# Kernel tuning notes

Measured on AMD Instinct MI355X. Metric: run time of the kernel, lower is better.

The kernel has to match this reference:

```python
import jax, jax.numpy as jnp
import numpy as np

B, Lc, Le, H, V = 128, 512, 512, 512, 128
PAD_IDX = 0  # ignore_index for cross entropy


def _lstm_cell(x, h, c, Wih, Whh, bih, bhh):
    # PyTorch gate order: i, f, g, o
    gates = x @ Wih.T + h @ Whh.T + bih + bhh
    i, f, g, o = jnp.split(gates, 4, axis=-1)
    c_new = jax.nn.sigmoid(f) * c + jax.nn.sigmoid(i) * jnp.tanh(g)
    h_new = jax.nn.sigmoid(o) * jnp.tanh(c_new)
    return h_new, c_new


def setup_inputs() -> dict:
    key = jax.random.key(0)
    ks = jax.random.split(key, 16)
    s = 0.05  # weight init scale
    inp = {
        "C": jax.random.normal(ks[0], (B, Lc, V), jnp.float32),
        "C_pad": jax.random.randint(ks[1], (B, Lc), 0, 2, jnp.int32).at[:, 0].set(0),
        "E": jax.random.randint(ks[2], (B, Le), 0, V, jnp.int32),
        "E_emb": jax.random.normal(ks[3], (B, Le, V), jnp.float32),
        # encoder LSTM (input V -> hidden H)
        "enc_Wih": s * jax.random.normal(ks[4], (4 * H, V), jnp.float32),
        "enc_Whh": s * jax.random.normal(ks[5], (4 * H, H), jnp.float32),
        "enc_bih": jnp.zeros((4 * H,), jnp.float32),
        "enc_bhh": jnp.zeros((4 * H,), jnp.float32),
        # decoder LSTMCell (input V+H -> hidden H); input is concat([E_emb_t, V_prev])
        "dec_Wih": s * jax.random.normal(ks[6], (4 * H, V + H), jnp.float32),
        "dec_Whh": s * jax.random.normal(ks[7], (4 * H, H), jnp.float32),
        "dec_bih": jnp.zeros((4 * H,), jnp.float32),
        "dec_bhh": jnp.zeros((4 * H,), jnp.float32),
        # attention_proj: Linear(H, H, bias=False)
        "att_W": s * jax.random.normal(ks[8], (H, H), jnp.float32),
        # output_proj: Linear(2H, H)
        "out_W": s * jax.random.normal(ks[9], (H, 2 * H), jnp.float32),
        "out_b": jnp.zeros((H,), jnp.float32),
        # vocab_proj: Linear(H, V)
        "voc_W": s * jax.random.normal(ks[10], (V, H), jnp.float32),
        "voc_b": jnp.zeros((V,), jnp.float32),
    }
    return inp


def reference(C, C_pad, E, E_emb, enc_Wih, enc_Whh, enc_bih, enc_bhh,
              dec_Wih, dec_Whh, dec_bih, dec_bhh, att_W, out_W, out_b,
              voc_W, voc_b):
    Bv = C.shape[0]
    Hh = enc_Whh.shape[1]

    # ---- encoder LSTM over compressed input ----
    def enc_step(carry, x_t):
        h, c = carry
        h, c = _lstm_cell(x_t, h, c, enc_Wih, enc_Whh, enc_bih, enc_bhh)
        return (h, c), h

    h0 = jnp.zeros((Bv, Hh), C.dtype)
    (hT, cT), enc_hs = jax.lax.scan(enc_step, (h0, h0), jnp.swapaxes(C, 0, 1))
    enc_hs = jnp.swapaxes(enc_hs, 0, 1)  # (B, Lc, H)
    pad = C_pad.astype(bool)              # (B, Lc)

    # ---- decoder loop (training mode, teacher forcing) ----
    def dec_step(carry, e_t):
        h, c, Vprev = carry
        x = jnp.concatenate([e_t, Vprev], axis=1)  # (B, V+H)
        h, c = _lstm_cell(x, h, c, dec_Wih, dec_Whh, dec_bih, dec_bhh)
        q = h @ att_W.T                                    # (B, H)
        scores = jnp.einsum('blh,bh->bl', enc_hs, q)       # (B, Lc)
        scores = jnp.where(pad, -jnp.inf, scores)
        d = jax.nn.softmax(scores, axis=1)
        attn = jnp.einsum('bl,blh->bh', d, enc_hs)         # (B, H)
        U = jnp.concatenate([h, attn], axis=1)             # (B, 2H)
        Vnew = U @ out_W.T + out_b                         # (B, H)
        # dropout treated as identity (eval-mode determinism)
        logits = jnp.tanh(Vnew) @ voc_W.T + voc_b          # (B, V)
        return (h, c, Vnew), logits

    Vinit = jnp.zeros((Bv, Hh), C.dtype)
    _, logits = jax.lax.scan(dec_step, (hT, cT, Vinit),
                             jnp.swapaxes(E_emb[:, :-1], 0, 1))
    logits = jnp.swapaxes(logits, 0, 1)  # (B, Le-1, V)

    # ---- cross entropy with ignore_index=PAD_IDX ----
    targets = E[:, 1:].astype(jnp.int32)
    logp = jax.nn.log_softmax(logits, axis=-1)
    nll = -jnp.take_along_axis(logp, targets[..., None], axis=-1)[..., 0]
    mask = (targets != PAD_IDX).astype(nll.dtype)
    loss = jnp.sum(nll * mask) / jnp.maximum(jnp.sum(mask), 1.0)
    return loss
```

## Files before the change

### kernel.cpp

```cpp
#include <hip/hip_runtime.h>
#include <hip/hip_bf16.h>


#define NWG 256
#define NT  256

typedef unsigned short u16;
typedef unsigned int   u32;
typedef unsigned long long u64;
typedef __attribute__((ext_vector_type(4))) float f4;
typedef __attribute__((ext_vector_type(8))) short s8;

constexpr int Bv=128, Lc=512, Le=512, Hd=512, Vc=128;
constexpr int KE=640, KD=1152;
constexpr int CAP = 144;
constexpr int SPN = 24;

constexpr size_t O_WENC = 8192;
constexpr size_t O_WDEC = O_WENC + (size_t)2048*KE*2;
constexpr size_t O_WDF  = O_WDEC + (size_t)2048*KD*2;
constexpr size_t O_ATWT = O_WDF  + (size_t)2048*KD*2;
constexpr size_t O_OUTW = O_ATWT + (size_t)512*512*2;
constexpr size_t O_VOCW = O_OUTW + (size_t)512*1024*2;
constexpr size_t O_BE   = O_VOCW + (size_t)128*512*2;
constexpr size_t O_BD   = O_BE + 8192;
constexpr size_t O_BDF  = O_BD + 8192;
constexpr size_t O_H    = O_BDF + 8192;
constexpr size_t O_TNH  = O_H + (size_t)2*128*512*2;
constexpr size_t O_PFX  = O_TNH + (size_t)2*128*512*2;
constexpr size_t O_CNT  = O_PFX + (size_t)128*512*4;
constexpr size_t O_PMS  = O_CNT + 512;
constexpr size_t O_PACC = O_PMS + 2048;
constexpr size_t O_REC  = O_PACC + (size_t)256*512*2;
constexpr size_t O_LOSS = O_REC + (size_t)2*128*2*4*4;
constexpr size_t O_ENC  = O_LOSS + 256;
constexpr size_t O_PSP  = O_ENC + (size_t)128*512*512*2;
constexpr size_t O_CST  = O_PSP + (size_t)256*SPN*512*2;

constexpr int SC       = CAP*1024;
constexpr int SM_BYTES = SC + 16384;

struct P {
  const float *C; const int *Cpad; const int *E; const float *Eemb;
  const float *eWih,*eWhh,*ebih,*ebhh;
  const float *dWih,*dWhh,*dbih,*dbhh;
  const float *attW,*outW,*outb,*vocW,*vocb;
  char* ws; float* out;
};

__device__ inline u16 f2bf(float x){
  u32 u = __float_as_uint(x);
  return (u16)((u + 0x7fffu + ((u>>16)&1u)) >> 16);
}
__device__ inline float bf2f(u16 b){ return __uint_as_float(((u32)b)<<16); }
__device__ inline float sigm(float x){ return 1.f/(1.f+expf(-x)); }
__device__ inline f4 MM(s8 a, s8 b, f4 c){
  return __builtin_amdgcn_mfma_f32_16x16x32_bf16(a, b, c, 0, 0, 0);
}
__device__ inline u64 ld64a(const void* p){
  return __hip_atomic_load((const u64*)p, __ATOMIC_RELAXED, __HIP_MEMORY_SCOPE_AGENT);
}
__device__ inline u32 ld32u(const void* p){
  return __hip_atomic_load((const u32*)p, __ATOMIC_RELAXED, __HIP_MEMORY_SCOPE_AGENT);
}
__device__ inline void st64a(void* p, u64 v){
  __hip_atomic_store((u64*)p, v, __ATOMIC_RELAXED, __HIP_MEMORY_SCOPE_AGENT);
}
__device__ inline void st32a(void* p, u32 v){
  __hip_atomic_store((u32*)p, v, __ATOMIC_RELAXED, __HIP_MEMORY_SCOPE_AGENT);
}
__device__ inline s8 ld16a(const void* p){
  union { u64 q[2]; s8 v; } u;
  u.q[0] = ld64a(p); u.q[1] = ld64a((const char*)p + 8);
  return u.v;
}
__device__ inline s8 cvt8(const float* p){
  f4 u = *(const f4*)p, v = *(const f4*)(p+4);
  s8 r;
  r[0]=(short)f2bf(u[0]); r[1]=(short)f2bf(u[1]); r[2]=(short)f2bf(u[2]); r[3]=(short)f2bf(u[3]);
  r[4]=(short)f2bf(v[0]); r[5]=(short)f2bf(v[1]); r[6]=(short)f2bf(v[2]); r[7]=(short)f2bf(v[3]);
  return r;
}
__device__ inline float wredmax(float v){
  #pragma unroll
  for (int m=32;m;m>>=1) v = fmaxf(v, __shfl_xor(v,m,64));
  return v;
}
__device__ inline float wredsum(float v){
  #pragma unroll
  for (int m=32;m;m>>=1) v += __shfl_xor(v,m,64);
  return v;
}

extern "C" __global__ void __launch_bounds__(NT,1) k_enc(P p)
{
  extern __shared__ char sm[];
  const int wg = blockIdx.x, tid = threadIdx.x;
  const int gt = wg*NT + tid;
  const int rg = wg >> 5, cg = wg & 31;

  char* ws = p.ws;
  u32*  slotA = (u32*)ws;
  u32*  slotR = (u32*)(ws + 1024 + rg*128);
  u16*  wenc = (u16*)(ws + O_WENC);
  u16*  wdec = (u16*)(ws + O_WDEC);
  u16*  wdf  = (u16*)(ws + O_WDF);
  u16*  atwt = (u16*)(ws + O_ATWT);
  u16*  outw = (u16*)(ws + O_OUTW);
  u16*  vocw = (u16*)(ws + O_VOCW);
  float* be  = (float*)(ws + O_BE);
  float* bd  = (float*)(ws + O_BD);
  float* bdf = (float*)(ws + O_BDF);
  u16*  hbf  = (u16*)(ws + O_H);
  u32*  pfx  = (u32*)(ws + O_PFX);
  u32*  cntp = (u32*)(ws + O_CNT);
  float* losp= (float*)(ws + O_LOSS);
  u16*  encc = (u16*)(ws + O_ENC);
  float* cstg= (float*)(ws + O_CST);

  u32 genA = 0, genG = 0;
  auto GBall = [&](){
    genA++;
    __syncthreads();
// ... 98 lines not shown
    int* padl = (int*)(sm + SC);
    for (int i = tid; i < 512; i += NT) padl[i] = p.Cpad[wg*512 + i];
    __syncthreads();
    if (tid == 0){
      u32 run = 0;
      for (int tt = 0; tt < 512; tt++){ pfx[wg*512+tt] = run; if (padl[tt] == 0) run++; }
      cntp[wg] = run;
    }
    __syncthreads();
  }
  GBall();

  const int l  = tid & 63, wv = tid >> 6;
  const int n2 = wv >> 1, k2 = wv & 1;
  const int kl = (l>>4) << 3;
  const int ar = rg*16 + (l&15);
  float cst = 0.f;

  const int gR0 = (n2*2+0)*512 + cg*16 + (l&15);
  const int gR1 = (n2*2+1)*512 + cg*16 + (l&15);

  for (int t = 0; t < Lc; t++){
    const u16* hold = hbf + (t&1)*Bv*Hd;
    u16* hnew       = hbf + ((t+1)&1)*Bv*Hd;
    s8 a[10];
    if (k2 == 0){
      #pragma unroll
      for (int ks = 4; ks < 10; ks++)
        a[ks] = ld16a(hold + (size_t)ar*Hd + (ks*32 + kl - 128));
      #pragma unroll
      for (int ks = 0; ks < 4; ks++)
        a[ks] = cvt8(p.C + ((size_t)ar*Lc + t)*Vc + ks*32 + kl);
    } else {
      #pragma unroll
      for (int ks = 0; ks < 10; ks++)
        a[ks] = ld16a(hold + (size_t)ar*Hd + (192 + ks*32 + kl));
    }
    f4 acc0 = {0,0,0,0}, acc1 = {0,0,0,0};
    #pragma unroll
    for (int ks = 0; ks < 10; ks++){
      int k = k2*320 + ks*32 + kl;
      acc0 = MM(a[ks], *(const s8*)(wenc + (size_t)gR0*KE + k), acc0);
      acc1 = MM(a[ks], *(const s8*)(wenc + (size_t)gR1*KE + k), acc1);
    }
    float* exch = (float*)(sm + SC);
    #pragma unroll
    for (int r = 0; r < 4; r++){
      int row = ((l>>4)<<2) + r;
      exch[((k2*4 + n2*2+0)*16 + row)*16 + (l&15)] = acc0[r];
      exch[((k2*4 + n2*2+1)*16 + row)*16 + (l&15)] = acc1[r];
    }
    __syncthreads();
    {
      int row = tid >> 4, u = tid & 15;
      int gb = cg*16 + u;
      float gi = exch[((0)*16+row)*16+u] + exch[((4)*16+row)*16+u] + be[0*512+gb];
      float gf = exch[((1)*16+row)*16+u] + exch[((5)*16+row)*16+u] + be[1*512+gb];
      float gg = exch[((2)*16+row)*16+u] + exch[((6)*16+row)*16+u] + be[2*512+gb];
      float go = exch[((3)*16+row)*16+u] + exch[((7)*16+row)*16+u] + be[3*512+gb];
      float fi = sigm(gi), ff = sigm(gf), fg = tanhf(gg), fo = sigm(go);
      cst = ff*cst + fi*fg;
      float hn = fo * tanhf(cst);
      int b = rg*16 + row;
      u32 hb = f2bf(hn);
      u32 nb = __shfl_xor((int)hb, 1, 64);
      if ((tid & 1) == 0){
        u32 pk = hb | (nb << 16);
        st32a(hnew + (size_t)b*Hd + gb, pk);
        if (p.Cpad[b*Lc + t] == 0){
          u32 pos = pfx[b*Lc + t];
          st32a(encc + ((size_t)b*Lc + pos)*Hd + gb, pk);
        }
      }
    }
    RGB();
  }

  {
    int row = tid >> 4, u = tid & 15;
    cstg[(size_t)(rg*16+row)*Hd + cg*16 + u] = cst;
  }
}

extern "C" __global__ void __launch_bounds__(NT,1) k_dec(P p)
{
  extern __shared__ char sm[];
  const int wg = blockIdx.x, tid = threadIdx.x;
  const int rg = wg >> 5, cg = wg & 31;

  char* ws = p.ws;
  u32*  slotA = (u32*)(ws + 2048);
  u32*  slotR = (u32*)(ws + 4096 + rg*128);
  u16*  wdec = (u16*)(ws + O_WDEC);
  u16*  wdf  = (u16*)(ws + O_WDF);
  u16*  atwt = (u16*)(ws + O_ATWT);
  u16*  outw = (u16*)(ws + O_OUTW);
  u16*  vocw = (u16*)(ws + O_VOCW);
  float* bd  = (float*)(ws + O_BD);
  float* bdf = (float*)(ws + O_BDF);
  u16*  hbf  = (u16*)(ws + O_H);
  u16*  tnhb = (u16*)(ws + O_TNH);
  u32*  cntp = (u32*)(ws + O_CNT);
  u64*  pms  = (u64*)(ws + O_PMS);
  u16*  pacc16 = (u16*)(ws + O_PACC);
  float* rec = (float*)(ws + O_REC);
  float* losp= (float*)(ws + O_LOSS);
  u16*  encc = (u16*)(ws + O_ENC);
  u16*  spl  = (u16*)(ws + O_PSP) + (size_t)wg*SPN*Hd;
  float* cstg= (float*)(ws + O_CST);

  u32 genA = 0, genG = 0;
  auto GBall = [&](){
    genA++;
    __syncthreads();
    if (tid == 0){
      __builtin_amdgcn_fence(__ATOMIC_RELEASE, "agent");
      st32a(slotA + wg, genA);
    }
    if (tid < 64){
      bool done = false;
      while (!done){
        u32 v0 = ld32u(slotA + tid);
        u32 v1 = ld32u(slotA + 64 + tid);
        u32 v2 = ld32u(slotA + 128 + tid);
        u32 v3 = ld32u(slotA + 192 + tid);
        done = __all((v0>=genA)&&(v1>=genA)&&(v2>=genA)&&(v3>=genA));
        if (!done) __builtin_amdgcn_s_sleep(4);
      }
      __builtin_amdgcn_fence(__ATOMIC_ACQUIRE, "agent");
    }
    __syncthreads();
  };
  auto RGB = [&](){
    genG++;
    __syncthreads();
    if (tid == 0) st32a(slotR + cg, genG);
    if (tid < 64){
      bool done = false;
      while (!done){
        u32 v = ld32u(slotR + (tid & 31));
        done = __all(v >= genG);
        if (!done) __builtin_amdgcn_s_sleep(2);
      }
      __builtin_amdgcn_fence(__ATOMIC_ACQUIRE, "workgroup");
    }
    __syncthreads();
  };

  const int l  = tid & 63, wv = tid >> 6;
  const int n2 = wv >> 1, k2 = wv & 1;
  const int kl = (l>>4) << 3;
  const int ar = rg*16 + (l&15);
  float accN = 0.f, accC = 0.f;

  float cst;
  {
    int row = tid >> 4, u = tid & 15;
    cst = cstg[(size_t)(rg*16+row)*Hd + cg*16 + u];
  }

  const int rowA = rg*16 + (cg >> 1), halfA = cg & 1;
  const int cnA = (int)cntp[rowA], c2A = cnA >> 1;
  const int loA = halfA ? c2A : 0;
  const int mynA = (halfA ? cnA : c2A) - loA;
  const int ncapA = mynA < CAP ? mynA : CAP;
  const int limA  = mynA < CAP+SPN ? mynA : CAP+SPN;
  u16* eP = (u16*)sm;

  auto CEREC = [&](int tl){
    u32* th16 = (u32*)(sm + SC + 11776);
    float* lgp = (float*)(sm + SC + 12800);
    float* lgh = (float*)(sm + SC + 13824);
    const u16* tb = tnhb + (size_t)(tl&1)*Bv*Hd + (size_t)rowA*Hd;
    th16[tid] = ld32u(tb + 2*tid);
    __syncthreads();
    {
      int v = tid & 63, ksl = tid >> 6;
      int gv = halfA*64 + v;
      const u16* wp = vocw + (size_t)gv*Hd + ksl*128;
      const u16* hp = (const u16*)th16 + ksl*128;
      float acc = 0.f;
      #pragma unroll 4
      for (int j = 0; j < 16; j++){
        s8 wv8 = *(const s8*)(wp + j*8);
        #pragma unroll
        for (int q = 0; q < 8; q++) acc += bf2f((u16)wv8[q]) * bf2f(hp[j*8+q]);
      }
      lgp[ksl*64 + v] = acc;
    }
    __syncthreads();
    if (tid < 64){
      int gv = halfA*64 + tid;
      float lv = lgp[tid] + lgp[64+tid] + lgp[128+tid] + lgp[192+tid] + p.vocb[gv];
      lgh[tid] = lv;
      float m = wredmax(lv);
      float s = wredsum(expf(lv - m));
      if (tid == 0){
        int tgt = p.E[rowA*Le + tl + 1];
        float tlg = (tgt >= halfA*64 && tgt < halfA*64+64) ? lgh[tgt - halfA*64] : 0.f;
        float* rp = rec + ((size_t)(tl&1)*256 + rowA*2 + halfA)*4;
        union { u64 q; float f[2]; } pk; pk.f[0]=m; pk.f[1]=s;
        st64a(rp, pk.q);
        st32a(rp+2, __float_as_uint(tlg));
      }
    }
    __syncthreads();
  };
  auto COMB = [&](int tl){
    int tgt = p.E[rowA*Le + tl + 1];
    if (tgt != 0){
      const float* rp = rec + ((size_t)(tl&1)*256 + rowA*2)*4;
      union { u64 q; float f[2]; } a, b;
      a.q = ld64a(rp); b.q = ld64a(rp+4);
      float tA = __uint_as_float(ld32u(rp+2)), tB = __uint_as_float(ld32u(rp+6));
      float M = fmaxf(a.f[0], b.f[0]);
      float S = a.f[1]*expf(a.f[0]-M) + b.f[1]*expf(b.f[0]-M);
      accN += logf(S) + M - (tA + tB);
      accC += 1.f;
    }
  };

  const int gR0 = (n2*2+0)*512 + cg*16 + (l&15);
  const int gR1 = (n2*2+1)*512 + cg*16 + (l&15);

  {
    const u16* erow = encc + ((size_t)rowA*Lc + loA)*Hd;
    for (int it = 0; it*16 < limA; it++){
      s8 afr[16];
      const u16* ap = erow + (size_t)(it*16 + (l&15))*Hd;
      #pragma unroll
      for (int ks = 0; ks < 16; ks++) afr[ks] = *(const s8*)(ap + ks*32 + kl);
      for (int ot = 0; ot < 8; ot++){
        int kout0 = wv*128 + ot*16;
        f4 acc = {0,0,0,0};
        #pragma unroll
        for (int ks = 0; ks < 16; ks++)
          acc = MM(afr[ks], *(const s8*)(atwt + (size_t)(kout0 + (l&15))*Hd + ks*32 + kl), acc);
        #pragma unroll
        for (int r = 0; r < 4; r++){
          int prow = it*16 + ((l>>4)<<2) + r;
          int pcol = kout0 + (l&15);
          if (prow < limA){
            u16 pv = f2bf(acc[r]);
            if (prow < CAP) eP[(size_t)prow*Hd + pcol] = pv;
            else            spl[(size_t)(prow-CAP)*Hd + pcol] = pv;
          }
        }
      }
    }
    __syncthreads();
  }

  float* exch = (float*)(sm + SC);
  float* vex  = (float*)(sm + SC + 8192);
  float* sc2  = (float*)(sm + SC + 12288);
  s8 aH[14];

  for (int t = 0; t < Le-1; t++){
    const u16* hold = hbf + (t&1)*Bv*Hd;
    u16* hnew       = hbf + ((t+1)&1)*Bv*Hd;

    if (t == 0){
      s8 a[10];
      #pragma unroll
      for (int ks = 0; ks < 10; ks++){
        int ke = (k2==0) ? ((ks<4) ? ks*32+kl : 640 + (ks-4)*32 + kl)
                         : (832 + ks*32 + kl);
        if (ke < 128) a[ks] = cvt8(p.Eemb + ((size_t)ar*Le + 0)*Vc + ke);
        else          a[ks] = ld16a(hold + (size_t)ar*Hd + (ke-640));
      }
      f4 acc0 = {0,0,0,0}, acc1 = {0,0,0,0};
      #pragma unroll
      for (int ks = 0; ks < 10; ks++){
        int ke = (k2==0) ? ((ks<4) ? ks*32+kl : 640 + (ks-4)*32 + kl)
                         : (832 + ks*32 + kl);
        acc0 = MM(a[ks], *(const s8*)(wdec + (size_t)gR0*KD + ke), acc0);
        acc1 = MM(a[ks], *(const s8*)(wdec + (size_t)gR1*KD + ke), acc1);
      }
      #pragma unroll
      for (int r = 0; r < 4; r++){
        int row = ((l>>4)<<2) + r;
        exch[((k2*4 + n2*2+0)*16 + row)*16 + (l&15)] = acc0[r];
        exch[((k2*4 + n2*2+1)*16 + row)*16 + (l&15)] = acc1[r];
      }
      __syncthreads();
      {
        int row = tid >> 4, u = tid & 15;
        int gb = cg*16 + u;
        float gi = exch[((0)*16+row)*16+u] + exch[((4)*16+row)*16+u] + bd[0*512+gb];
        float gf = exch[((1)*16+row)*16+u] + exch[((5)*16+row)*16+u] + bd[1*512+gb];
        float gg = exch[((2)*16+row)*16+u] + exch[((6)*16+row)*16+u] + bd[2*512+gb];
        float go = exch[((3)*16+row)*16+u] + exch[((7)*16+row)*16+u] + bd[3*512+gb];
        float fi = sigm(gi), ff = sigm(gf), fg = tanhf(gg), fo = sigm(go);
        cst = ff*cst + fi*fg;
        float hn = fo * tanhf(cst);
        u32 hb = f2bf(hn);
        u32 nb = __shfl_xor((int)hb, 1, 64);
        if ((tid & 1) == 0)
          st32a(hnew + (size_t)(rg*16+row)*Hd + gb, hb | (nb << 16));
      }
    } else {
      if (tid < 16){
        union { u64 q; float f[2]; } uA, uB;
        uA.q = ld64a(pms + (rg*16+tid)*2 + 0);
        uB.q = ld64a(pms + (rg*16+tid)*2 + 1);
        float M = fmaxf(uA.f[0], uB.f[0]);
        float eA = (uA.f[0] > -1e29f) ? expf(uA.f[0]-M) : 0.f;
        float eB = (uB.f[0] > -1e29f) ? expf(uB.f[0]-M) : 0.f;
        float den = uA.f[1]*eA + uB.f[1]*eB;
        sc2[tid*2]   = eA/den;
        sc2[tid*2+1] = eB/den;
      }
      __syncthreads();
      const int colc = cg*16 + (l&15);
      if (k2 == 0){
        s8 a[18];
        #pragma unroll
        for (int ks = 4; ks < 18; ks++) a[ks] = aH[ks-4];
        #pragma unroll
        for (int ks = 0; ks < 4; ks++)
          a[ks] = cvt8(p.Eemb + ((size_t)ar*Le + t)*Vc + ks*32 + kl);
        f4 acc0 = {0,0,0,0}, acc1 = {0,0,0,0}, vac = {0,0,0,0};
        #pragma unroll
        for (int ks = 0; ks < 18; ks++){
          int k = ks*32 + kl;
          acc0 = MM(a[ks], *(const s8*)(wdf + (size_t)gR0*KD + k), acc0);
          acc1 = MM(a[ks], *(const s8*)(wdf + (size_t)gR1*KD + k), acc1);
          int ck = ks - 4;
          if (ck >= 0 && ((ck & 1) == n2))
            vac = MM(a[ks], *(const s8*)(outw + (size_t)colc*1024 + ck*32 + kl), vac);
        }
        #pragma unroll
        for (int r = 0; r < 4; r++){
          int row = ((l>>4)<<2) + r;
          exch[((n2*2+0)*16 + row)*16 + (l&15)] = acc0[r];
          exch[((n2*2+1)*16 + row)*16 + (l&15)] = acc1[r];
          vex[wv*256 + row*16 + (l&15)] = vac[r];
        }
      } else {
        const u16* pA = pacc16 + (size_t)(ar*2+0)*Hd;
        const u16* pB = pacc16 + (size_t)(ar*2+1)*Hd;
        s8 h0f = aH[0], h1f = aH[1];
        f4 acc0 = {0,0,0,0}, acc1 = {0,0,0,0};
        f4 aA0 = {0,0,0,0}, aA1 = {0,0,0,0}, aB0 = {0,0,0,0}, aB1 = {0,0,0,0};
        f4 vH = {0,0,0,0}, vA = {0,0,0,0}, vB = {0,0,0,0};
        acc0 = MM(h0f, *(const s8*)(wdf + (size_t)gR0*KD + 576 + kl), acc0);
        acc1 = MM(h0f, *(const s8*)(wdf + (size_t)gR1*KD + 576 + kl), acc1);
        acc0 = MM(h1f, *(const s8*)(wdf + (size_t)gR0*KD + 608 + kl), acc0);
        acc1 = MM(h1f, *(const s8*)(wdf + (size_t)gR1*KD + 608 + kl), acc1);
        {
          s8 hf = (n2 == 0) ? h0f : h1f;
          vH = MM(hf, *(const s8*)(outw + (size_t)colc*1024 + (14+n2)*32 + kl), vH);
        }
        #pragma unroll
        for (int hb = 0; hb < 2; hb++){
          s8 pf[8];
          #pragma unroll
          for (int j = 0; j < 8; j++)
            pf[j] = ld16a(pA + (hb*8+j)*32 + kl);
          #pragma unroll
          for (int j = 0; j < 8; j++){
            int c = hb*8 + j;
            int k = 640 + c*32 + kl;
            aA0 = MM(pf[j], *(const s8*)(wdf + (size_t)gR0*KD + k), aA0);
            aA1 = MM(pf[j], *(const s8*)(wdf + (size_t)gR1*KD + k), aA1);
            if (((16 + c) & 1) == n2)
              vA = MM(pf[j], *(const s8*)(outw + (size_t)colc*1024 + (16+c)*32 + kl), vA);
          }
        }
        #pragma unroll
        for (int hb = 0; hb < 2; hb++){
          s8 pf[8];
          #pragma unroll
          for (int j = 0; j < 8; j++)
            pf[j] = ld16a(pB + (hb*8+j)*32 + kl);
          #pragma unroll
          for (int j = 0; j < 8; j++){
            int c = hb*8 + j;
            int k = 640 + c*32 + kl;
            aB0 = MM(pf[j], *(const s8*)(wdf + (size_t)gR0*KD + k), aB0);
            aB1 = MM(pf[j], *(const s8*)(wdf + (size_t)gR1*KD + k), aB1);
            if (((16 + c) & 1) == n2)
              vB = MM(pf[j], *(const s8*)(outw + (size_t)colc*1024 + (16+c)*32 + kl), vB);
          }
        }
        #pragma unroll
        for (int r = 0; r < 4; r++){
          int row = ((l>>4)<<2) + r;
          float sAr = sc2[row*2], sBr = sc2[row*2+1];
          exch[((4 + n2*2+0)*16 + row)*16 + (l&15)] = acc0[r] + sAr*aA0[r] + sBr*aB0[r];
          exch[((4 + n2*2+1)*16 + row)*16 + (l&15)] = acc1[r] + sAr*aA1[r] + sBr*aB1[r];
          vex[wv*256 + row*16 + (l&15)] = vH[r] + sAr*vA[r] + sBr*vB[r];
        }
      }
      __syncthreads();
      {
        int row = tid >> 4, u = tid & 15;
        int gb = cg*16 + u;
        float gi = exch[((0)*16+row)*16+u] + exch[((4)*16+row)*16+u] + bdf[0*512+gb];
        float gf = exch[((1)*16+row)*16+u] + exch[((5)*16+row)*16+u] + bdf[1*512+gb];
        float gg = exch[((2)*16+row)*16+u] + exch[((6)*16+row)*16+u] + bdf[2*512+gb];
        float go = exch[((3)*16+row)*16+u] + exch[((7)*16+row)*16+u] + bdf[3*512+gb];
        float fi = sigm(gi), ff = sigm(gf), fg = tanhf(gg), fo = sigm(go);
        cst = ff*cst + fi*fg;
        float hn = fo * tanhf(cst);
        u32 hb = f2bf(hn);
        u32 nb = __shfl_xor((int)hb, 1, 64);
        if ((tid & 1) == 0)
          st32a(hnew + (size_t)(rg*16+row)*Hd + gb, hb | (nb << 16));
        float v = vex[row*16+u] + vex[256+row*16+u] + vex[512+row*16+u]
                + vex[768+row*16+u] + p.outb[gb];
        u32 tb2 = f2bf(tanhf(v));
        u32 tn2 = __shfl_xor((int)tb2, 1, 64);
        if ((tid & 1) == 0){
          u16* tnw = tnhb + (size_t)((t-1)&1)*Bv*Hd;
          st32a(tnw + (size_t)(rg*16+row)*Hd + gb, tb2 | (tn2 << 16));
        }
      }
    }
    RGB();

    {
      const int ne = limA, ncap = ncapA;
      float* hld = (float*)(sm + SC);
      float* scl = (float*)(sm + SC + 2048);
      float* red = (float*)(sm + SC + 2816);
      float* part= (float*)(sm + SC + 3584);
      {
        u32 hw = ld32u(hnew + (size_t)rowA*Hd + 2*tid);
        int c0 = 2*tid, c1 = c0+1;
        hld[(c0&15)*32 + (c0>>4)] = bf2f((u16)(hw & 0xffffu));
        hld[(c1&15)*32 + (c1>>4)] = bf2f((u16)(hw >> 16));
      }
      __syncthreads();
      const int pg8 = tid >> 5, ln = tid & 31;
      int i = pg8;
      for (; i < ncap; i += 8){
        const u16* e = eP + (size_t)i*Hd + ln*16;
        s8 ev0 = *(const s8*)(e);
        s8 ev1 = *(const s8*)(e+8);
        float s = 0.f;
        #pragma unroll
        for (int j=0;j<8;j++) s += bf2f((u16)ev0[j]) * hld[j*32+ln];
        #pragma unroll
        for (int j=0;j<8;j++) s += bf2f((u16)ev1[j]) * hld[(j+8)*32+ln];
        #pragma unroll
        for (int m=1;m<32;m<<=1) s += __shfl_xor(s, m, 64);
        if (ln == 0) scl[i] = s;
      }
      for (; i < ne; i += 8){
        const u16* e = spl + (size_t)(i-CAP)*Hd + ln*16;
        s8 ev0 = *(const s8*)(e);
        s8 ev1 = *(const s8*)(e+8);
        float s = 0.f;
        #pragma unroll
        for (int j=0;j<8;j++) s += bf2f((u16)ev0[j]) * hld[j*32+ln];
        #pragma unroll
        for (int j=0;j<8;j++) s += bf2f((u16)ev1[j]) * hld[(j+8)*32+ln];
        #pragma unroll
        for (int m=1;m<32;m<<=1) s += __shfl_xor(s, m, 64);
        if (ln == 0) scl[i] = s;
      }
      __syncthreads();
      float mloc = -1e30f;
      for (int i2 = tid; i2 < ne; i2 += NT) mloc = fmaxf(mloc, scl[i2]);
      mloc = wredmax(mloc);
      if ((tid&63)==0) red[tid>>6] = mloc;
      __syncthreads();
      float M = fmaxf(fmaxf(red[0],red[1]), fmaxf(red[2],red[3]));
      __syncthreads();
      float sloc = 0.f;
      for (int i2 = tid; i2 < ne; i2 += NT){ float w = expf(scl[i2]-M); scl[i2]=w; sloc += w; }
      sloc = wredsum(sloc);
      if ((tid&63)==0) red[tid>>6] = sloc;
      __syncthreads();
      float S = red[0]+red[1]+red[2]+red[3];
      float a8[8] = {0,0,0,0,0,0,0,0};
      const u16* eb2 = encc + ((size_t)rowA*Lc + loA)*Hd + l*8;
      int ii = wv;
      for (; ii + 28 < ne; ii += 32){
        s8 e0 = *(const s8*)(eb2 + (size_t)(ii    )*Hd);
        s8 e1 = *(const s8*)(eb2 + (size_t)(ii+ 4)*Hd);
        s8 e2 = *(const s8*)(eb2 + (size_t)(ii+ 8)*Hd);
        s8 e3 = *(const s8*)(eb2 + (size_t)(ii+12)*Hd);
        s8 e4 = *(const s8*)(eb2 + (size_t)(ii+16)*Hd);
        s8 e5 = *(const s8*)(eb2 + (size_t)(ii+20)*Hd);
        s8 e6 = *(const s8*)(eb2 + (size_t)(ii+24)*Hd);
        s8 e7 = *(const s8*)(eb2 + (size_t)(ii+28)*Hd);
        float w0=scl[ii], w1=scl[ii+4], w2=scl[ii+8], w3=scl[ii+12];
        float w4=scl[ii+16], w5=scl[ii+20], w6=scl[ii+24], w7=scl[ii+28];
        #pragma unroll
        for (int j=0;j<8;j++) a8[j] += w0*bf2f((u16)e0[j]) + w1*bf2f((u16)e1[j])
                                    + w2*bf2f((u16)e2[j]) + w3*bf2f((u16)e3[j])
                                    + w4*bf2f((u16)e4[j]) + w5*bf2f((u16)e5[j])
                                    + w6*bf2f((u16)e6[j]) + w7*bf2f((u16)e7[j]);
      }
      for (; ii < ne; ii += 4){
        s8 e0 = *(const s8*)(eb2 + (size_t)ii*Hd);
        float w0 = scl[ii];
        #pragma unroll
        for (int j=0;j<8;j++) a8[j] += w0*bf2f((u16)e0[j]);
      }
      { f4 v0 = {a8[0],a8[1],a8[2],a8[3]}, v1 = {a8[4],a8[5],a8[6],a8[7]};
        *(f4*)(part + wv*512 + l*8)     = v0;
        *(f4*)(part + wv*512 + l*8 + 4) = v1; }
      __syncthreads();
      {
        int h0 = 2*tid;
        float a0 = part[h0] + part[512+h0] + part[1024+h0] + part[1536+h0];
        float a1 = part[h0+1] + part[512+h0+1] + part[1024+h0+1] + part[1536+h0+1];
        st32a(pacc16 + (size_t)(rowA*2+halfA)*Hd + h0, (u32)f2bf(a0) | ((u32)f2bf(a1) << 16));
        if (tid == 0){
          union { u64 q; float f[2]; } pk; pk.f[0]=M; pk.f[1]=S;
          st64a(pms + rowA*2 + halfA, pk.q);
        }
      }
      __syncthreads();
      if (t >= 1) CEREC(t-1);
      if (t >= 2 && halfA == 0 && tid == 0) COMB(t-2);
      if (t < Le-2){
        if (k2 == 0){
          #pragma unroll
          for (int ks = 4; ks < 18; ks++)
            aH[ks-4] = ld16a(hnew + (size_t)ar*Hd + (ks*32 + kl - 128));
        } else {
          aH[0] = ld16a(hnew + (size_t)ar*Hd + (448 + kl));
          aH[1] = ld16a(hnew + (size_t)ar*Hd + (480 + kl));
        }
      }
    }
    RGB();
  }

  const int TL = Le-2;
  {
    if (tid < 16){
      union { u64 q; float f[2]; } uA, uB;
      uA.q = ld64a(pms + (rg*16+tid)*2 + 0);
      uB.q = ld64a(pms + (rg*16+tid)*2 + 1);
      float M = fmaxf(uA.f[0], uB.f[0]);
      float eA = (uA.f[0] > -1e29f) ? expf(uA.f[0]-M) : 0.f;
      float eB = (uB.f[0] > -1e29f) ? expf(uB.f[0]-M) : 0.f;
      float den = uA.f[1]*eA + uB.f[1]*eB;
      sc2[tid*2]   = eA/den;
      sc2[tid*2+1] = eB/den;
    }
    __syncthreads();
    const float scA = sc2[(l&15)*2], scB = sc2[(l&15)*2+1];
    const u16* h5 = hbf + (size_t)((TL+1)&1)*Bv*Hd;
    const u16* pA = pacc16 + (size_t)(ar*2+0)*Hd;
    const u16* pB = pacc16 + (size_t)(ar*2+1)*Hd;
    const int colc = cg*16 + (l&15);
    f4 vac = {0,0,0,0};
    #pragma unroll
    for (int j = 0; j < 8; j++){
      int kv = k2*16 + j*2 + n2;
      s8 af;
      if (kv < 16) af = ld16a(h5 + (size_t)ar*Hd + kv*32 + kl);
      else {
        s8 va = ld16a(pA + (kv-16)*32 + kl);
        s8 vb = ld16a(pB + (kv-16)*32 + kl);
        #pragma unroll
        for (int q = 0; q < 8; q++)
          af[q] = (short)f2bf(scA*bf2f((u16)va[q]) + scB*bf2f((u16)vb[q]));
      }
      vac = MM(af, *(const s8*)(outw + (size_t)colc*1024 + kv*32 + kl), vac);
    }
    #pragma unroll
    for (int r = 0; r < 4; r++)
      vex[wv*256 + (((l>>4)<<2)+r)*16 + (l&15)] = vac[r];
    __syncthreads();
    {
      int row = tid >> 4, u = tid & 15;
      int gb = cg*16 + u;
      float v = vex[row*16+u] + vex[256+row*16+u] + vex[512+row*16+u]
              + vex[768+row*16+u] + p.outb[gb];
      u32 tb2 = f2bf(tanhf(v));
      u32 tn2 = __shfl_xor((int)tb2, 1, 64);
      if ((tid & 1) == 0){
        u16* tnw = tnhb + (size_t)(TL&1)*Bv*Hd;
        st32a(tnw + (size_t)(rg*16+row)*Hd + gb, tb2 | (tn2 << 16));
      }
    }
  }
  RGB();
  {
    CEREC(TL);
    if (halfA == 0 && tid == 0) COMB(TL-1);
  }
  RGB();
  {
    if (halfA == 0 && tid == 0){
      COMB(TL);
      atomicAdd(losp + 0, accN);
      atomicAdd(losp + 1, accC);
    }
  }
  GBall();
  if (wg == 0 && tid == 0) p.out[0] = losp[0] / fmaxf(losp[1], 1.f);
}

extern "C" void kernel_launch(void* const* d_in, const int* in_sizes, int n_in,
                              void* d_out, int out_size, void* d_ws, size_t ws_size,
                              hipStream_t stream)
{
  hipFuncSetAttribute(reinterpret_cast<const void*>(k_enc),
                      hipFuncAttributeMaxDynamicSharedMemorySize, SM_BYTES);
  hipFuncSetAttribute(reinterpret_cast<const void*>(k_dec),
                      hipFuncAttributeMaxDynamicSharedMemorySize, SM_BYTES);
  hipMemsetAsync(d_ws, 0, 8192, stream);

  P prm;
  prm.C    = (const float*)d_in[0];
  prm.Cpad = (const int*)  d_in[1];
  prm.E    = (const int*)  d_in[2];
  prm.Eemb = (const float*)d_in[3];
  prm.eWih = (const float*)d_in[4];
  prm.eWhh = (const float*)d_in[5];
  prm.ebih = (const float*)d_in[6];
  prm.ebhh = (const float*)d_in[7];
  prm.dWih = (const float*)d_in[8];
  prm.dWhh = (const float*)d_in[9];
  prm.dbih = (const float*)d_in[10];
  prm.dbhh = (const float*)d_in[11];
  prm.attW = (const float*)d_in[12];
  prm.outW = (const float*)d_in[13];
  prm.outb = (const float*)d_in[14];
  prm.vocW = (const float*)d_in[15];
  prm.vocb = (const float*)d_in[16];
  prm.ws   = (char*)d_ws;
  prm.out  = (float*)d_out;

  k_enc<<<dim3(NWG), dim3(NT), SM_BYTES, stream>>>(prm);
  k_dec<<<dim3(NWG), dim3(NT), SM_BYTES, stream>>>(prm);
}
```

Baseline: 21.57 ms.

## Split decoder across 512 workgroups with 4-way attention partitioning per row

The decoder kernel now launches 512 persistent workgroups (two per CU via launch_bounds) instead of 256. Each row-group covers 8 batch rows instead of 16, and the attention over encoder states for each row is split four ways instead of two. The per-workgroup LDS cache of encoder projections shrinks to fit two blocks per CU. The partial softmax, attention and cross-entropy combines are widened to merge four partials. This spreads the attention and vocab work over more CUs, at the cost of a grid barrier that polls 512 slots, redundant MFMA tiles where only 8 of 16 rows are valid, and more spill to global memory.

```diff
diff --git a/kernel.cpp b/kernel.cpp
--- a/kernel.cpp
+++ b/kernel.cpp
@@ -4,6 +4,7 @@
 
 #define NWG 256
 #define NT  256
+#define NWG2 512
 
 typedef unsigned short u16;
 typedef unsigned int   u32;
@@ -13,8 +14,8 @@
 
 constexpr int Bv=128, Lc=512, Le=512, Hd=512, Vc=128;
 constexpr int KE=640, KD=1152;
-constexpr int CAP = 144;
-constexpr int SPN = 24;
+constexpr int CAP2 = 60;
+constexpr int SPN2 = 24;
 
 constexpr size_t O_WENC = 8192;
 constexpr size_t O_WDEC = O_WENC + (size_t)2048*KE*2;
@@ -30,15 +31,17 @@
 constexpr size_t O_PFX  = O_TNH + (size_t)2*128*512*2;
 constexpr size_t O_CNT  = O_PFX + (size_t)128*512*4;
 constexpr size_t O_PMS  = O_CNT + 512;
-constexpr size_t O_PACC = O_PMS + 2048;
-constexpr size_t O_REC  = O_PACC + (size_t)256*512*2;
-constexpr size_t O_LOSS = O_REC + (size_t)2*128*2*4*4;
+constexpr size_t O_PACC = O_PMS + 4096;
+constexpr size_t O_REC  = O_PACC + (size_t)128*4*512*2;
+constexpr size_t O_LOSS = O_REC + 16384;
 constexpr size_t O_ENC  = O_LOSS + 256;
 constexpr size_t O_PSP  = O_ENC + (size_t)128*512*512*2;
-constexpr size_t O_CST  = O_PSP + (size_t)256*SPN*512*2;
-
-constexpr int SC       = CAP*1024;
+constexpr size_t O_CST  = O_PSP + (size_t)NWG2*SPN2*512*2;
+
+constexpr int SC       = 144*1024;
 constexpr int SM_BYTES = SC + 16384;
+constexpr int SC2       = CAP2*1024;
+constexpr int SM2_BYTES = SC2 + 16384;
 
 struct P {
   const float *C; const int *Cpad; const int *E; const float *Eemb;
@@ -303,15 +306,15 @@
   }
 }
 
-extern "C" __global__ void __launch_bounds__(NT,1) k_dec(P p)
+extern "C" __global__ void __launch_bounds__(NT,2) k_dec(P p)
 {
   extern __shared__ char sm[];
   const int wg = blockIdx.x, tid = threadIdx.x;
-  const int rg = wg >> 5, cg = wg & 31;
+  const int rgx = wg >> 5, cg = wg & 31;
 
   char* ws = p.ws;
   u32*  slotA = (u32*)(ws + 2048);
-  u32*  slotR = (u32*)(ws + 4096 + rg*128);
+  u32*  slotR = (u32*)(ws + 4096 + rgx*128);
   u16*  wdec = (u16*)(ws + O_WDEC);
   u16*  wdf  = (u16*)(ws + O_WDF);
   u16*  atwt = (u16*)(ws + O_ATWT);
@@ -327,7 +330,7 @@
   float* rec = (float*)(ws + O_REC);
   float* losp= (float*)(ws + O_LOSS);
   u16*  encc = (u16*)(ws + O_ENC);
-  u16*  spl  = (u16*)(ws + O_PSP) + (size_t)wg*SPN*Hd;
+  u16*  spl  = (u16*)(ws + O_PSP) + (size_t)wg*SPN2*Hd;
   float* cstg= (float*)(ws + O_CST);
 
   u32 genA = 0, genG = 0;
@@ -341,11 +344,11 @@
     if (tid < 64){
       bool done = false;
       while (!done){
-        u32 v0 = ld32u(slotA + tid);
-        u32 v1 = ld32u(slotA + 64 + tid);
-        u32 v2 = ld32u(slotA + 128 + tid);
-        u32 v3 = ld32u(slotA + 192 + tid);
-        done = __all((v0>=genA)&&(v1>=genA)&&(v2>=genA)&&(v3>=genA));
+        bool ok = true;
+        #pragma unroll
+        for (int i = 0; i < 8; i++)
+          ok = ok && (ld32u(slotA + tid + 64*i) >= genA);
+        done = __all(ok);
         if (!done) __builtin_amdgcn_s_sleep(4);
       }
       __builtin_amdgcn_fence(__ATOMIC_ACQUIRE, "agent");
@@ -371,55 +374,62 @@
   const int l  = tid & 63, wv = tid >> 6;
   const int n2 = wv >> 1, k2 = wv & 1;
   const int kl = (l>>4) << 3;
-  const int ar = rg*16 + (l&15);
+  const int ar = rgx*8 + (l&7);
   float accN = 0.f, accC = 0.f;
 
-  float cst;
-  {
+  float cst = 0.f;
+  if (tid < 128){
     int row = tid >> 4, u = tid & 15;
-    cst = cstg[(size_t)(rg*16+row)*Hd + cg*16 + u];
-  }
-
-  const int rowA = rg*16 + (cg >> 1), halfA = cg & 1;
-  const int cnA = (int)cntp[rowA], c2A = cnA >> 1;
-  const int loA = halfA ? c2A : 0;
-  const int mynA = (halfA ? cnA : c2A) - loA;
-  const int ncapA = mynA < CAP ? mynA : CAP;
-  const int limA  = mynA < CAP+SPN ? mynA : CAP+SPN;
+    cst = cstg[(size_t)(rgx*8+row)*Hd + cg*16 + u];
+  }
+
+  const int rowA = rgx*8 + (cg >> 2), q4 = cg & 3;
+  const int cnA = (int)cntp[rowA];
+  const int loA = (cnA * q4) >> 2;
+  const int hiA = (cnA * (q4+1)) >> 2;
+  const int mynA = hiA - loA;
+  const int ncapA = mynA < CAP2 ? mynA : CAP2;
+  const int limA  = mynA < CAP2+SPN2 ? mynA : CAP2+SPN2;
   u16* eP = (u16*)sm;
 
   auto CEREC = [&](int tl){
-    u32* th16 = (u32*)(sm + SC + 11776);
-    float* lgp = (float*)(sm + SC + 12800);
-    float* lgh = (float*)(sm + SC + 13824);
+    u32* th16 = (u32*)(sm + SC2 + 11776);
+    float* lgp = (float*)(sm + SC2 + 12800);
+    float* lgh = (float*)(sm + SC2 + 13824);
     const u16* tb = tnhb + (size_t)(tl&1)*Bv*Hd + (size_t)rowA*Hd;
     th16[tid] = ld32u(tb + 2*tid);
     __syncthreads();
     {
-      int v = tid & 63, ksl = tid >> 6;
-      int gv = halfA*64 + v;
-      const u16* wp = vocw + (size_t)gv*Hd + ksl*128;
-      const u16* hp = (const u16*)th16 + ksl*128;
+      int v = tid & 31, ksl = tid >> 5;
+      int gv = q4*32 + v;
+      const u16* wp = vocw + (size_t)gv*Hd + ksl*64;
+      const u16* hp = (const u16*)th16 + ksl*64;
       float acc = 0.f;
-      #pragma unroll 4
-      for (int j = 0; j < 16; j++){
+      #pragma unroll
+      for (int j = 0; j < 8; j++){
         s8 wv8 = *(const s8*)(wp + j*8);
         #pragma unroll
         for (int q = 0; q < 8; q++) acc += bf2f((u16)wv8[q]) * bf2f(hp[j*8+q]);
       }
-      lgp[ksl*64 + v] = acc;
-    }
-    __syncthreads();
-    if (tid < 64){
-      int gv = halfA*64 + tid;
-      float lv = lgp[tid] + lgp[64+tid] + lgp[128+tid] + lgp[192+tid] + p.vocb[gv];
+      lgp[ksl*32 + v] = acc;
+    }
+    __syncthreads();
+    if (tid < 32){
+      int gv = q4*32 + tid;
+      float lv = p.vocb[gv];
+      #pragma unroll
+      for (int s2 = 0; s2 < 8; s2++) lv += lgp[s2*32 + tid];
       lgh[tid] = lv;
-      float m = wredmax(lv);
-      float s = wredsum(expf(lv - m));
+      float m = lv, s;
+      #pragma unroll
+      for (int mk=16;mk;mk>>=1) m = fmaxf(m, __shfl_xor(m, mk, 64));
+      s = expf(lv - m);
+      #pragma unroll
+      for (int mk=16;mk;mk>>=1) s += __shfl_xor(s, mk, 64);
       if (tid == 0){
         int tgt = p.E[rowA*Le + tl + 1];
-        float tlg = (tgt >= halfA*64 && tgt < halfA*64+64) ? lgh[tgt - halfA*64] : 0.f;
-        float* rp = rec + ((size_t)(tl&1)*256 + rowA*2 + halfA)*4;
+        float tlg = (tgt >= q4*32 && tgt < q4*32+32) ? lgh[tgt - q4*32] : 0.f;
+        float* rp = rec + ((size_t)(tl&1)*2048 + rowA*16 + q4*4);
         union { u64 q; float f[2]; } pk; pk.f[0]=m; pk.f[1]=s;
         st64a(rp, pk.q);
         st32a(rp+2, __float_as_uint(tlg));
@@ -430,13 +440,21 @@
   auto COMB = [&](int tl){
     int tgt = p.E[rowA*Le + tl + 1];
     if (tgt != 0){
-      const float* rp = rec + ((size_t)(tl&1)*256 + rowA*2)*4;
-      union { u64 q; float f[2]; } a, b;
-      a.q = ld64a(rp); b.q = ld64a(rp+4);
-      float tA = __uint_as_float(ld32u(rp+2)), tB = __uint_as_float(ld32u(rp+6));
-      float M = fmaxf(a.f[0], b.f[0]);
-      float S = a.f[1]*expf(a.f[0]-M) + b.f[1]*expf(b.f[0]-M);
-      accN += logf(S) + M - (tA + tB);
+      const float* rp = rec + ((size_t)(tl&1)*2048 + rowA*16);
+      float m[4], s[4], tsum = 0.f;
+      #pragma unroll
+      for (int q = 0; q < 4; q++){
+        union { u64 u; float f[2]; } a;
+        a.u = ld64a(rp + q*4);
+        m[q] = a.f[0]; s[q] = a.f[1];
+        tsum += __uint_as_float(ld32u(rp + q*4 + 2));
+      }
+      float M = fmaxf(fmaxf(m[0],m[1]), fmaxf(m[2],m[3]));
+      float S = 0.f;
+      #pragma unroll
+      for (int q = 0; q < 4; q++)
+        S += (m[q] > -1e29f) ? s[q]*expf(m[q]-M) : 0.f;
+      accN += logf(S) + M - tsum;
       accC += 1.f;
     }
   };
@@ -463,8 +481,8 @@
           int pcol = kout0 + (l&15);
           if (prow < limA){
             u16 pv = f2bf(acc[r]);
-            if (prow < CAP) eP[(size_t)prow*Hd + pcol] = pv;
-            else            spl[(size_t)(prow-CAP)*Hd + pcol] = pv;
+            if (prow < CAP2) eP[(size_t)prow*Hd + pcol] = pv;
+            else             spl[(size_t)(prow-CAP2)*Hd + pcol] = pv;
           }
         }
       }
@@ -472,9 +490,9 @@
     __syncthreads();
   }
 
-  float* exch = (float*)(sm + SC);
-  float* vex  = (float*)(sm + SC + 8192);
-  float* sc2  = (float*)(sm + SC + 12288);
+  float* exch = (float*)(sm + SC2);
+  float* vex  = (float*)(sm + SC2 + 8192);
+  float* sc4  = (float*)(sm + SC2 + 12288);
   s8 aH[14];
 
   for (int t = 0; t < Le-1; t++){
@@ -505,7 +523,7 @@
         exch[((k2*4 + n2*2+1)*16 + row)*16 + (l&15)] = acc1[r];
       }
       __syncthreads();
-      {
+      if (tid < 128){
         int row = tid >> 4, u = tid & 15;
         int gb = cg*16 + u;
         float gi = exch[((0)*16+row)*16+u] + exch[((4)*16+row)*16+u] + bd[0*512+gb];
@@ -518,19 +536,26 @@
         u32 hb = f2bf(hn);
         u32 nb = __shfl_xor((int)hb, 1, 64);
         if ((tid & 1) == 0)
-          st32a(hnew + (size_t)(rg*16+row)*Hd + gb, hb | (nb << 16));
+          st32a(hnew + (size_t)(rgx*8+row)*Hd + gb, hb | (nb << 16));
       }
     } else {
-      if (tid < 16){
-        union { u64 q; float f[2]; } uA, uB;
-        uA.q = ld64a(pms + (rg*16+tid)*2 + 0);
-        uB.q = ld64a(pms + (rg*16+tid)*2 + 1);
-        float M = fmaxf(uA.f[0], uB.f[0]);
-        float eA = (uA.f[0] > -1e29f) ? expf(uA.f[0]-M) : 0.f;
-        float eB = (uB.f[0] > -1e29f) ? expf(uB.f[0]-M) : 0.f;
-        float den = uA.f[1]*eA + uB.f[1]*eB;
-        sc2[tid*2]   = eA/den;
-        sc2[tid*2+1] = eB/den;
+      if (tid < 8){
+        float m[4], s[4];
+        #pragma unroll
+        for (int q = 0; q < 4; q++){
+          union { u64 u; float f[2]; } a;
+          a.u = ld64a(pms + (rgx*8+tid)*4 + q);
+          m[q] = a.f[0]; s[q] = a.f[1];
+        }
+        float M = fmaxf(fmaxf(m[0],m[1]), fmaxf(m[2],m[3]));
+        float e[4]; float den = 0.f;
+        #pragma unroll
+        for (int q = 0; q < 4; q++){
+          e[q] = (m[q] > -1e29f) ? expf(m[q]-M) : 0.f;
+          den += s[q]*e[q];
+        }
+        #pragma unroll
+        for (int q = 0; q < 4; q++) sc4[tid*4+q] = e[q]/den;
       }
       __syncthreads();
       const int colc = cg*16 + (l&15);
@@ -559,12 +584,15 @@
           vex[wv*256 + row*16 + (l&15)] = vac[r];
         }
       } else {
-        const u16* pA = pacc16 + (size_t)(ar*2+0)*Hd;
-        const u16* pB = pacc16 + (size_t)(ar*2+1)*Hd;
+        const u16* pQ0 = pacc16 + (size_t)(ar*4+0)*Hd;
+        const u16* pQ1 = pacc16 + (size_t)(ar*4+1)*Hd;
+        const u16* pQ2 = pacc16 + (size_t)(ar*4+2)*Hd;
+        const u16* pQ3 = pacc16 + (size_t)(ar*4+3)*Hd;
         s8 h0f = aH[0], h1f = aH[1];
         f4 acc0 = {0,0,0,0}, acc1 = {0,0,0,0};
-        f4 aA0 = {0,0,0,0}, aA1 = {0,0,0,0}, aB0 = {0,0,0,0}, aB1 = {0,0,0,0};
-        f4 vH = {0,0,0,0}, vA = {0,0,0,0}, vB = {0,0,0,0};
+        f4 aA0={0,0,0,0},aA1={0,0,0,0},aB0={0,0,0,0},aB1={0,0,0,0};
+        f4 aC0={0,0,0,0},aC1={0,0,0,0},aD0={0,0,0,0},aD1={0,0,0,0};
+        f4 vH={0,0,0,0},vA={0,0,0,0},vB={0,0,0,0},vC={0,0,0,0},vD={0,0,0,0};
         acc0 = MM(h0f, *(const s8*)(wdf + (size_t)gR0*KD + 576 + kl), acc0);
         acc1 = MM(h0f, *(const s8*)(wdf + (size_t)gR1*KD + 576 + kl), acc1);
         acc0 = MM(h1f, *(const s8*)(wdf + (size_t)gR0*KD + 608 + kl), acc0);
@@ -574,48 +602,40 @@
           vH = MM(hf, *(const s8*)(outw + (size_t)colc*1024 + (14+n2)*32 + kl), vH);
         }
         #pragma unroll
-        for (int hb = 0; hb < 2; hb++){
-          s8 pf[8];
-          #pragma unroll
-          for (int j = 0; j < 8; j++)
-            pf[j] = ld16a(pA + (hb*8+j)*32 + kl);
-          #pragma unroll
-          for (int j = 0; j < 8; j++){
-            int c = hb*8 + j;
-            int k = 640 + c*32 + kl;
-            aA0 = MM(pf[j], *(const s8*)(wdf + (size_t)gR0*KD + k), aA0);
-            aA1 = MM(pf[j], *(const s8*)(wdf + (size_t)gR1*KD + k), aA1);
-            if (((16 + c) & 1) == n2)
-              vA = MM(pf[j], *(const s8*)(outw + (size_t)colc*1024 + (16+c)*32 + kl), vA);
+        for (int c = 0; c < 16; c++){
+          int k = 640 + c*32 + kl;
+          s8 p0 = ld16a(pQ0 + c*32 + kl);
+          s8 p1 = ld16a(pQ1 + c*32 + kl);
+          s8 p2 = ld16a(pQ2 + c*32 + kl);
+          s8 p3 = ld16a(pQ3 + c*32 + kl);
+          s8 b0 = *(const s8*)(wdf + (size_t)gR0*KD + k);
+          s8 b1 = *(const s8*)(wdf + (size_t)gR1*KD + k);
+          aA0 = MM(p0,b0,aA0); aA1 = MM(p0,b1,aA1);
+          aB0 = MM(p1,b0,aB0); aB1 = MM(p1,b1,aB1);
+          aC0 = MM(p2,b0,aC0); aC1 = MM(p2,b1,aC1);
+          aD0 = MM(p3,b0,aD0); aD1 = MM(p3,b1,aD1);
+          if (((16 + c) & 1) == n2){
+            s8 bo = *(const s8*)(outw + (size_t)colc*1024 + (16+c)*32 + kl);
+            vA = MM(p0,bo,vA); vB = MM(p1,bo,vB);
+            vC = MM(p2,bo,vC); vD = MM(p3,bo,vD);
           }
         }
         #pragma unroll
-        for (int hb = 0; hb < 2; hb++){
-          s8 pf[8];
-          #pragma unroll
-          for (int j = 0; j < 8; j++)
-            pf[j] = ld16a(pB + (hb*8+j)*32 + kl);
-          #pragma unroll
-          for (int j = 0; j < 8; j++){
-            int c = hb*8 + j;
-            int k = 640 + c*32 + kl;
-            aB0 = MM(pf[j], *(const s8*)(wdf + (size_t)gR0*KD + k), aB0);
-            aB1 = MM(pf[j], *(const s8*)(wdf + (size_t)gR1*KD + k), aB1);
-            if (((16 + c) & 1) == n2)
-              vB = MM(pf[j], *(const s8*)(outw + (size_t)colc*1024 + (16+c)*32 + kl), vB);
-          }
-        }
-        #pragma unroll
         for (int r = 0; r < 4; r++){
-          int row = ((l>>4)<<2) + r;
-          float sAr = sc2[row*2], sBr = sc2[row*2+1];
-          exch[((4 + n2*2+0)*16 + row)*16 + (l&15)] = acc0[r] + sAr*aA0[r] + sBr*aB0[r];
-          exch[((4 + n2*2+1)*16 + row)*16 + (l&15)] = acc1[r] + sAr*aA1[r] + sBr*aB1[r];
-          vex[wv*256 + row*16 + (l&15)] = vH[r] + sAr*vA[r] + sBr*vB[r];
-        }
-      }
-      __syncthreads();
-      {
+          int row16 = ((l>>4)<<2) + r;
+          int rw = row16 & 7;
+          float sA = sc4[rw*4+0], sB = sc4[rw*4+1];
+          float sC = sc4[rw*4+2], sD = sc4[rw*4+3];
+          exch[((4 + n2*2+0)*16 + row16)*16 + (l&15)] =
+            acc0[r] + sA*aA0[r] + sB*aB0[r] + sC*aC0[r] + sD*aD0[r];
+          exch[((4 + n2*2+1)*16 + row16)*16 + (l&15)] =
+            acc1[r] + sA*aA1[r] + sB*aB1[r] + sC*aC1[r] + sD*aD1[r];
+          vex[wv*256 + row16*16 + (l&15)] =
+            vH[r] + sA*vA[r] + sB*vB[r] + sC*vC[r] + sD*vD[r];
+        }
+      }
+      __syncthreads();
+      if (tid < 128){
         int row = tid >> 4, u = tid & 15;
         int gb = cg*16 + u;
         float gi = exch[((0)*16+row)*16+u] + exch[((4)*16+row)*16+u] + bdf[0*512+gb];
@@ -628,14 +648,14 @@
         u32 hb = f2bf(hn);
         u32 nb = __shfl_xor((int)hb, 1, 64);
         if ((tid & 1) == 0)
-          st32a(hnew + (size_t)(rg*16+row)*Hd + gb, hb | (nb << 16));
+          st32a(hnew + (size_t)(rgx*8+row)*Hd + gb, hb | (nb << 16));
         float v = vex[row*16+u] + vex[256+row*16+u] + vex[512+row*16+u]
                 + vex[768+row*16+u] + p.outb[gb];
         u32 tb2 = f2bf(tanhf(v));
         u32 tn2 = __shfl_xor((int)tb2, 1, 64);
         if ((tid & 1) == 0){
           u16* tnw = tnhb + (size_t)((t-1)&1)*Bv*Hd;
-          st32a(tnw + (size_t)(rg*16+row)*Hd + gb, tb2 | (tn2 << 16));
+          st32a(tnw + (size_t)(rgx*8+row)*Hd + gb, tb2 | (tn2 << 16));
         }
       }
     }
@@ -643,10 +663,10 @@
 
     {
       const int ne = limA, ncap = ncapA;
-      float* hld = (float*)(sm + SC);
-      float* scl = (float*)(sm + SC + 2048);
-      float* red = (float*)(sm + SC + 2816);
-      float* part= (float*)(sm + SC + 3584);
+      float* hld = (float*)(sm + SC2);
+      float* scl = (float*)(sm + SC2 + 2048);
+      float* red = (float*)(sm + SC2 + 2816);
+      float* part= (float*)(sm + SC2 + 3584);
       {
         u32 hw = ld32u(hnew + (size_t)rowA*Hd + 2*tid);
         int c0 = 2*tid, c1 = c0+1;
@@ -670,7 +690,7 @@
         if (ln == 0) scl[i] = s;
       }
       for (; i < ne; i += 8){
-        const u16* e = spl + (size_t)(i-CAP)*Hd + ln*16;
+        const u16* e = spl + (size_t)(i-CAP2)*Hd + ln*16;
         s8 ev0 = *(const s8*)(e);
         s8 ev1 = *(const s8*)(e+8);
         float s = 0.f;
@@ -699,22 +719,15 @@
       float a8[8] = {0,0,0,0,0,0,0,0};
       const u16* eb2 = encc + ((size_t)rowA*Lc + loA)*Hd + l*8;
       int ii = wv;
-      for (; ii + 28 < ne; ii += 32){
-        s8 e0 = *(const s8*)(eb2 + (size_t)(ii    )*Hd);
+      for (; ii + 12 < ne; ii += 16){
+        s8 e0 = *(const s8*)(eb2 + (size_t)(ii   )*Hd);
         s8 e1 = *(const s8*)(eb2 + (size_t)(ii+ 4)*Hd);
         s8 e2 = *(const s8*)(eb2 + (size_t)(ii+ 8)*Hd);
         s8 e3 = *(const s8*)(eb2 + (size_t)(ii+12)*Hd);
-        s8 e4 = *(const s8*)(eb2 + (size_t)(ii+16)*Hd);
-        s8 e5 = *(const s8*)(eb2 + (size_t)(ii+20)*Hd);
-        s8 e6 = *(const s8*)(eb2 + (size_t)(ii+24)*Hd);
-        s8 e7 = *(const s8*)(eb2 + (size_t)(ii+28)*Hd);
         float w0=scl[ii], w1=scl[ii+4], w2=scl[ii+8], w3=scl[ii+12];
-        float w4=scl[ii+16], w5=scl[ii+20], w6=scl[ii+24], w7=scl[ii+28];
         #pragma unroll
         for (int j=0;j<8;j++) a8[j] += w0*bf2f((u16)e0[j]) + w1*bf2f((u16)e1[j])
-                                    + w2*bf2f((u16)e2[j]) + w3*bf2f((u16)e3[j])
-                                    + w4*bf2f((u16)e4[j]) + w5*bf2f((u16)e5[j])
-                                    + w6*bf2f((u16)e6[j]) + w7*bf2f((u16)e7[j]);
+                                    + w2*bf2f((u16)e2[j]) + w3*bf2f((u16)e3[j]);
       }
       for (; ii < ne; ii += 4){
         s8 e0 = *(const s8*)(eb2 + (size_t)ii*Hd);
@@ -730,15 +743,15 @@
         int h0 = 2*tid;
         float a0 = part[h0] + part[512+h0] + part[1024+h0] + part[1536+h0];
         float a1 = part[h0+1] + part[512+h0+1] + part[1024+h0+1] + part[1536+h0+1];
-        st32a(pacc16 + (size_t)(rowA*2+halfA)*Hd + h0, (u32)f2bf(a0) | ((u32)f2bf(a1) << 16));
+        st32a(pacc16 + (size_t)(rowA*4+q4)*Hd + h0, (u32)f2bf(a0) | ((u32)f2bf(a1) << 16));
         if (tid == 0){
           union { u64 q; float f[2]; } pk; pk.f[0]=M; pk.f[1]=S;
-          st64a(pms + rowA*2 + halfA, pk.q);
+          st64a(pms + rowA*4 + q4, pk.q);
         }
       }
       __syncthreads();
       if (t >= 1) CEREC(t-1);
-      if (t >= 2 && halfA == 0 && tid == 0) COMB(t-2);
+      if (t >= 2 && q4 == 0 && tid == 0) COMB(t-2);
       if (t < Le-2){
         if (k2 == 0){
           #pragma unroll
@@ -755,22 +768,32 @@
 
   const int TL = Le-2;
   {
-    if (tid < 16){
-      union { u64 q; float f[2]; } uA, uB;
-      uA.q = ld64a(pms + (rg*16+tid)*2 + 0);
-      uB.q = ld64a(pms + (rg*16+tid)*2 + 1);
-      float M = fmaxf(uA.f[0], uB.f[0]);
-      float eA = (uA.f[0] > -1e29f) ? expf(uA.f[0]-M) : 0.f;
-      float eB = (uB.f[0] > -1e29f) ? expf(uB.f[0]-M) : 0.f;
-      float den = uA.f[1]*eA + uB.f[1]*eB;
-      sc2[tid*2]   = eA/den;
-      sc2[tid*2+1] = eB/den;
-    }
-    __syncthreads();
-    const float scA = sc2[(l&15)*2], scB = sc2[(l&15)*2+1];
+    if (tid < 8){
+      float m[4], s[4];
+      #pragma unroll
+      for (int q = 0; q < 4; q++){
+        union { u64 u; float f[2]; } a;
+        a.u = ld64a(pms + (rgx*8+tid)*4 + q);
+        m[q] = a.f[0]; s[q] = a.f[1];
+      }
+      float M = fmaxf(fmaxf(m[0],m[1]), fmaxf(m[2],m[3]));
+      float e[4]; float den = 0.f;
+      #pragma unroll
+      for (int q = 0; q < 4; q++){
+        e[q] = (m[q] > -1e29f) ? expf(m[q]-M) : 0.f;
+        den += s[q]*e[q];
+      }
+      #pragma unroll
+      for (int q = 0; q < 4; q++) sc4[tid*4+q] = e[q]/den;
+    }
+    __syncthreads();
     const u16* h5 = hbf + (size_t)((TL+1)&1)*Bv*Hd;
-    const u16* pA = pacc16 + (size_t)(ar*2+0)*Hd;
-    const u16* pB = pacc16 + (size_t)(ar*2+1)*Hd;
+    const u16* pQ0 = pacc16 + (size_t)(ar*4+0)*Hd;
+    const u16* pQ1 = pacc16 + (size_t)(ar*4+1)*Hd;
+    const u16* pQ2 = pacc16 + (size_t)(ar*4+2)*Hd;
+    const u16* pQ3 = pacc16 + (size_t)(ar*4+3)*Hd;
+    const float sA = sc4[(l&7)*4+0], sB = sc4[(l&7)*4+1];
+    const float sC = sc4[(l&7)*4+2], sD = sc4[(l&7)*4+3];
     const int colc = cg*16 + (l&15);
     f4 vac = {0,0,0,0};
     #pragma unroll
@@ -779,11 +802,14 @@
       s8 af;
       if (kv < 16) af = ld16a(h5 + (size_t)ar*Hd + kv*32 + kl);
       else {
-        s8 va = ld16a(pA + (kv-16)*32 + kl);
-        s8 vb = ld16a(pB + (kv-16)*32 + kl);
+        s8 v0 = ld16a(pQ0 + (kv-16)*32 + kl);
+        s8 v1 = ld16a(pQ1 + (kv-16)*32 + kl);
+        s8 v2 = ld16a(pQ2 + (kv-16)*32 + kl);
+        s8 v3 = ld16a(pQ3 + (kv-16)*32 + kl);
         #pragma unroll
         for (int q = 0; q < 8; q++)
-          af[q] = (short)f2bf(scA*bf2f((u16)va[q]) + scB*bf2f((u16)vb[q]));
+          af[q] = (short)f2bf(sA*bf2f((u16)v0[q]) + sB*bf2f((u16)v1[q])
+                            + sC*bf2f((u16)v2[q]) + sD*bf2f((u16)v3[q]));
       }
       vac = MM(af, *(const s8*)(outw + (size_t)colc*1024 + kv*32 + kl), vac);
     }
@@ -791,7 +817,7 @@
     for (int r = 0; r < 4; r++)
       vex[wv*256 + (((l>>4)<<2)+r)*16 + (l&15)] = vac[r];
     __syncthreads();
-    {
+    if (tid < 128){
       int row = tid >> 4, u = tid & 15;
       int gb = cg*16 + u;
       float v = vex[row*16+u] + vex[256+row*16+u] + vex[512+row*16+u]
@@ -800,18 +826,18 @@
       u32 tn2 = __shfl_xor((int)tb2, 1, 64);
       if ((tid & 1) == 0){
         u16* tnw = tnhb + (size_t)(TL&1)*Bv*Hd;
-        st32a(tnw + (size_t)(rg*16+row)*Hd + gb, tb2 | (tn2 << 16));
+        st32a(tnw + (size_t)(rgx*8+row)*Hd + gb, tb2 | (tn2 << 16));
       }
     }
   }
   RGB();
   {
     CEREC(TL);
-    if (halfA == 0 && tid == 0) COMB(TL-1);
+    if (q4 == 0 && tid == 0) COMB(TL-1);
   }
   RGB();
   {
-    if (halfA == 0 && tid == 0){
+    if (q4 == 0 && tid == 0){
       COMB(TL);
       atomicAdd(losp + 0, accN);
       atomicAdd(losp + 1, accC);
@@ -828,7 +854,7 @@
   hipFuncSetAttribute(reinterpret_cast<const void*>(k_enc),
                       hipFuncAttributeMaxDynamicSharedMemorySize, SM_BYTES);
   hipFuncSetAttribute(reinterpret_cast<const void*>(k_dec),
-                      hipFuncAttributeMaxDynamicSharedMemorySize, SM_BYTES);
+                      hipFuncAttributeMaxDynamicSharedMemorySize, SM2_BYTES);
   hipMemsetAsync(d_ws, 0, 8192, stream);
 
   P prm;
@@ -852,6 +878,6 @@
   prm.ws   = (char*)d_ws;
   prm.out  = (float*)d_out;
 
-  k_enc<<<dim3(NWG), dim3(NT), SM_BYTES, stream>>>(prm);
-  k_dec<<<dim3(NWG), dim3(NT), SM_BYTES, stream>>>(prm);
-}
+  k_enc<<<dim3(NWG),  dim3(NT), SM_BYTES,  stream>>>(prm);
+  k_dec<<<dim3(NWG2), dim3(NT), SM2_BYTES, stream>>>(prm);
+}
```

Measured after the change: 27.60 ms. 1.28x slower.
